# Optimization experiments

Hardware: AMD Instinct MI355X
Metric: run time of the kernel (lower is better)

Reference implementation:

```python
import jax, jax.numpy as jnp
import numpy as np

EPS = 1e-5
NUM_HEADS = 4


def setup_inputs() -> dict:
    key = jax.random.key(0)
    ks = jax.random.split(key, 10)
    B, C, H, W = 16, 512, 32, 32
    s = 1.0 / np.sqrt(C)
    x = jax.random.normal(ks[0], (B, C, H, W), dtype=jnp.float32)
    gn_weight = jnp.ones((C,), jnp.float32)
    gn_bias = jnp.zeros((C,), jnp.float32)
    wq = jax.random.uniform(ks[1], (C, C), jnp.float32, -s, s)
    bq = jax.random.uniform(ks[2], (C,), jnp.float32, -s, s)
    wk = jax.random.uniform(ks[3], (C, C), jnp.float32, -s, s)
    bk = jax.random.uniform(ks[4], (C,), jnp.float32, -s, s)
    wv = jax.random.uniform(ks[5], (C, C), jnp.float32, -s, s)
    bv = jax.random.uniform(ks[6], (C,), jnp.float32, -s, s)
    wo = jax.random.uniform(ks[7], (C, C), jnp.float32, -s, s)
    bo = jax.random.uniform(ks[8], (C,), jnp.float32, -s, s)
    return dict(x=x, gn_weight=gn_weight, gn_bias=gn_bias, wq=wq, bq=bq,
                wk=wk, bk=bk, wv=wv, bv=bv, wo=wo, bo=bo)


def reference(x, gn_weight, gn_bias, wq, bq, wk, bk, wv, bv, wo, bo):
    B, C, H, W = x.shape
    head_size = C // NUM_HEADS

    # GroupNorm(num_groups=1): normalize over (C,H,W) per batch element
    mean = jnp.mean(x, axis=(1, 2, 3), keepdims=True)
    var = jnp.var(x, axis=(1, 2, 3), keepdims=True)
    xn = (x - mean) / jnp.sqrt(var + EPS)
    xn = xn * gn_weight[None, :, None, None] + gn_bias[None, :, None, None]

    # (B, C, H, W) -> (B, S, C) with S = H*W
    seq = xn.reshape(B, C, H * W).transpose(0, 2, 1)

    def heads(y):  # (B, S, C) -> (B, nh, S, hd)
        return y.reshape(B, H * W, NUM_HEADS, head_size).transpose(0, 2, 1, 3)

    q = heads(seq @ wq.T + bq)
    k = heads(seq @ wk.T + bk)
    v = heads(seq @ wv.T + bv)

    scores = jnp.einsum('bhqd,bhkd->bhqk', q, k) / np.sqrt(head_size).astype(np.float32)
    attn = jax.nn.softmax(scores, axis=-1)
    out = jnp.einsum('bhqk,bhkd->bhqd', attn, v)  # (B, nh, S, hd)

    out = out.transpose(0, 2, 1, 3).reshape(B, H * W, C)
    out = out @ wo.T + bo
    out = out.transpose(0, 2, 1).reshape(B, C, H, W)
    return out + x
```

## Files before the change

### kernel.cpp

```cpp
#include <hip/hip_runtime.h>
#include <stdint.h>

#define B_  16
#define C_  512
#define S_  1024
#define NH  4
#define HD  128
#define BS  (B_*S_)

typedef __attribute__((ext_vector_type(8))) short   short8;
typedef __attribute__((ext_vector_type(4))) float   f32x4;
typedef __attribute__((ext_vector_type(4))) unsigned int uint4v;

__device__ __forceinline__ unsigned short f2bf(float f) {
    unsigned u = __float_as_uint(f);
    unsigned r = (u + 0x7fffu + ((u >> 16) & 1u)) >> 16;
    return (unsigned short)r;
}

__device__ __forceinline__ unsigned cvt_pk_bf16(float a, float b) {
    unsigned r;
    asm("v_cvt_pk_bf16_f32 %0, %1, %2" : "=v"(r) : "v"(a), "v"(b));
    return r;
}

__global__ void gn_partial(const float* __restrict__ x, float* __restrict__ part) {
    int b = blockIdx.x, chunk = blockIdx.y;
    const float4* xb = (const float4*)(x + (size_t)b * C_ * S_);
    int base = chunk * 4096 + threadIdx.x;
    float s = 0.f, ss = 0.f;
#pragma unroll
    for (int i = 0; i < 16; ++i) {
        float4 v = xb[base + i * 256];
        s  += v.x + v.y + v.z + v.w;
        ss += v.x*v.x + v.y*v.y + v.z*v.z + v.w*v.w;
    }
    for (int off = 32; off; off >>= 1) { s += __shfl_down(s, off); ss += __shfl_down(ss, off); }
    __shared__ float red[2][4];
    int wv = threadIdx.x >> 6;
    if ((threadIdx.x & 63) == 0) { red[0][wv] = s; red[1][wv] = ss; }
    __syncthreads();
    if (threadIdx.x == 0) {
        s  = red[0][0] + red[0][1] + red[0][2] + red[0][3];
        ss = red[1][0] + red[1][1] + red[1][2] + red[1][3];
        part[(b*32 + chunk)*2 + 0] = s;
        part[(b*32 + chunk)*2 + 1] = ss;
    }
}

__global__ void gn_apply_t(const float* __restrict__ x, const float* __restrict__ part,
                           const float* __restrict__ gw, const float* __restrict__ gb,
                           unsigned short* __restrict__ seq) {
    int st = blockIdx.x, ct = blockIdx.y, b = blockIdx.z;
    float s1 = 0.f, s2 = 0.f;
#pragma unroll
    for (int i = 0; i < 32; ++i) { s1 += part[(b*32+i)*2]; s2 += part[(b*32+i)*2+1]; }
    const float invN = 1.0f / (float)(C_ * S_);
    float mean = s1 * invN;
    float var  = s2 * invN - mean * mean;
    float rstd = rsqrtf(var + 1e-5f);

    __shared__ unsigned short tile[64][72];
    int c0 = ct * 64, s0 = st * 64;
    const float* xb = x + ((size_t)b * C_ + c0) * S_ + s0;
    int tr = threadIdx.x >> 4, tj = (threadIdx.x & 15) * 4;
#pragma unroll
    for (int p = 0; p < 4; ++p) {
        int i = tr + p * 16;
        float w  = gw[c0 + i];
        float bb = gb[c0 + i];
        float4 v = *(const float4*)(xb + (size_t)i * S_ + tj);
        tile[i][tj+0] = f2bf((v.x - mean) * rstd * w + bb);
        tile[i][tj+1] = f2bf((v.y - mean) * rstd * w + bb);
        tile[i][tj+2] = f2bf((v.z - mean) * rstd * w + bb);
        tile[i][tj+3] = f2bf((v.w - mean) * rstd * w + bb);
    }
    __syncthreads();
    int j  = threadIdx.x >> 2;
    int cc = (threadIdx.x & 3) * 16;
    unsigned short tmp[16] __attribute__((aligned(16)));
#pragma unroll
    for (int i = 0; i < 16; ++i) tmp[i] = tile[cc + i][j];
    unsigned short* dst = seq + ((size_t)(b * S_ + s0 + j)) * C_ + c0 + cc;
    *(uint4v*)dst       = *(uint4v*)tmp;
    *(uint4v*)(dst + 8) = *(uint4v*)(tmp + 8);
}

__global__ void cvt_w(const float* __restrict__ wq, const float* __restrict__ wk,
                      const float* __restrict__ wv, const float* __restrict__ wo,
                      unsigned short* __restrict__ wqkv, unsigned short* __restrict__ wobf) {
    int m = blockIdx.y;
    const float* src = (m == 0) ? wq : (m == 1) ? wk : (m == 2) ? wv : wo;
    unsigned short* dst = (m < 3) ? (wqkv + (size_t)m * C_ * C_) : wobf;
    int i = blockIdx.x * 256 + threadIdx.x;
    float4 v = ((const float4*)src)[i];
    unsigned short o[4] __attribute__((aligned(8)));
    o[0] = f2bf(v.x); o[1] = f2bf(v.y); o[2] = f2bf(v.z); o[3] = f2bf(v.w);
    *(unsigned long long*)(dst + (size_t)i * 4) = *(unsigned long long*)o;
}

__device__ __forceinline__ void gemm128_bt(const unsigned short* __restrict__ Ab,
                                           const unsigned short* __restrict__ Bb,
                                           const int K,
                                           unsigned short* lA, unsigned short* lB,
                                           f32x4 acc[4][4]) {
    const int t = threadIdx.x;
    const int w = t >> 6, l = t & 63;
    const int wr = (w >> 1) * 64, wc = (w & 1) * 64;
    const int lrow = l & 15;
    const int lk8  = (l >> 4) * 8;
#pragma unroll
    for (int mi = 0; mi < 4; ++mi)
#pragma unroll
        for (int ni = 0; ni < 4; ++ni)
            acc[mi][ni] = (f32x4){0.f, 0.f, 0.f, 0.f};

    for (int kt = 0; kt < K; kt += 64) {
#pragma unroll
        for (int j = 0; j < 4; ++j) {
            const int lin = j * 256 + t;
            const int row = lin >> 3, ch = lin & 7;
            __builtin_amdgcn_global_load_lds(
                (const __attribute__((address_space(1))) unsigned int*)(Ab + (size_t)row * K + kt + ch * 8),
                (__attribute__((address_space(3))) unsigned int*)(lA + (size_t)(j * 256 + w * 64) * 8),
                16, 0, 0);
        }
#pragma unroll
        for (int j = 0; j < 4; ++j) {
            const int lin = j * 256 + t;
            const int row = lin >> 3, ch = lin & 7;
            __builtin_amdgcn_global_load_lds(
                (const __attribute__((address_space(1))) unsigned int*)(Bb + (size_t)row * K + kt + ch * 8),
                (__attribute__((address_space(3))) unsigned int*)(lB + (size_t)(j * 256 + w * 64) * 8),
                16, 0, 0);
        }
        __syncthreads();
#pragma unroll
        for (int kk = 0; kk < 2; ++kk) {
            short8 af[4], bf[4];
            const int ko = lk8 + kk * 32;
#pragma unroll
            for (int mi = 0; mi < 4; ++mi)
                af[mi] = *(const short8*)&lA[(size_t)(wr + mi * 16 + lrow) * 64 + ko];
#pragma unroll
            for (int ni = 0; ni < 4; ++ni)
                bf[ni] = *(const short8*)&lB[(size_t)(wc + ni * 16 + lrow) * 64 + ko];
#pragma unroll
            for (int mi = 0; mi < 4; ++mi)
#pragma unroll
                for (int ni = 0; ni < 4; ++ni)
                    acc[mi][ni] = __builtin_amdgcn_mfma_f32_16x16x32_bf16(af[mi], bf[ni], acc[mi][ni], 0, 0, 0);
        }
        __syncthreads();
    }
}

__global__ __launch_bounds__(256) void qkv_gemm(
        const unsigned short* __restrict__ seq, const unsigned short* __restrict__ wqkv,
        const float* __restrict__ bq, const float* __restrict__ bk, const float* __restrict__ bv,
        unsigned short* __restrict__ qb, unsigned short* __restrict__ kb, unsigned short* __restrict__ vtb) {
    __shared__ unsigned short sbuf[128 * 136];
    unsigned short* lA = sbuf;
    unsigned short* lB = sbuf + 128 * 64;
    int mb = blockIdx.x, nb = blockIdx.y;
    f32x4 acc[4][4];
    gemm128_bt(seq + (size_t)mb * 128 * C_, wqkv + (size_t)nb * 128 * C_, C_, lA, lB, acc);

    int mat = nb >> 2;
    int cb = (nb & 3) * 128;
    int w = threadIdx.x >> 6, l = threadIdx.x & 63;
    int l15 = l & 15, g = l >> 4;
    int wr = (w >> 1) * 64, wc = (w & 1) * 64;

    if (mat < 2) {
        const float* bias = (mat == 0) ? bq : bk;
        unsigned short* out = (mat == 0) ? qb : kb;
        float oscale = (mat == 0) ? 0.12751879523087253f : 1.0f;
#pragma unroll
        for (int mi = 0; mi < 4; ++mi)
#pragma unroll
            for (int ni = 0; ni < 4; ++ni)
#pragma unroll
                for (int r = 0; r < 4; ++r) {
                    int m = mb * 128 + wr + mi * 16 + g * 4 + r;
                    int c = cb + wc + ni * 16 + l15;
                    int b = m >> 10, s = m & 1023;
                    int h = c >> 7,  d = c & 127;
                    float v = (acc[mi][ni][r] + bias[c]) * oscale;
                    out[(((size_t)(b * NH + h) * S_) + s) * HD + d] = f2bf(v);
                }
    } else {
        int b  = mb >> 3;
        int s0 = (mb & 7) * 128;
        int h  = nb & 3;
#pragma unroll
        for (int mi = 0; mi < 4; ++mi)
#pragma unroll
            for (int ni = 0; ni < 4; ++ni) {
                int dloc = wc + ni * 16 + l15;
                int mloc = wr + mi * 16 + g * 4;
                float bia = bv[h * 128 + dloc];
#pragma unroll
                for (int r = 0; r < 4; ++r)
                    sbuf[dloc * 136 + mloc + r] = f2bf(acc[mi][ni][r] + bia);
            }
        __syncthreads();
        unsigned short* dst = vtb + ((size_t)(b * NH + h)) * HD * S_ + s0;
#pragma unroll
        for (int p = 0; p < 8; ++p) {
            int idx = p * 256 + threadIdx.x;
            int d = idx >> 4, cc = (idx & 15) * 8;
            short8 vv = *(const short8*)&sbuf[d * 136 + cc];
            *(short8*)(dst + (size_t)d * S_ + cc) = vv;
        }
    }
}

__global__ __launch_bounds__(256) void flash_attn(
        const unsigned short* __restrict__ q, const unsigned short* __restrict__ k,
        const unsigned short* __restrict__ vt, unsigned short* __restrict__ o) {
    int bh = blockIdx.x, qblk = blockIdx.y;
    int t = threadIdx.x, w = t >> 6, l = t & 63;
    int l15 = l & 15, g = l >> 4;
    int swz = (l15 & 7) << 1;
    __shared__ unsigned short lK[2][64 * 128];
    __shared__ unsigned short lV[2][128 * 64];
    __shared__ unsigned short lP[4][32 * 64];

    const size_t bh_base = (size_t)bh * S_ * HD;
    int q0 = qblk * 128 + w * 32;

    short8 qa[4], qb_[4];
    const unsigned short* qp = q + bh_base + (size_t)(q0 + l15) * HD + g * 8;
#pragma unroll
    for (int kc = 0; kc < 4; ++kc) {
        qa[kc]  = *(const short8*)(qp + kc * 32);
        qb_[kc] = *(const short8*)(qp + 16 * HD + kc * 32);
    }

    short8 onesf;
#pragma unroll
    for (int i = 0; i < 8; ++i) onesf[i] = (short)0x3F80;

    int ko[4];
#pragma unroll
    for (int nb = 0; nb < 4; ++nb) {
        int row = nb * 16 + l15;
        ko[nb] = row * 256 + ((g ^ row) & 7) * 16;
    }
    int vo[8];
#pragma unroll
    for (int dn = 0; dn < 8; ++dn) {
        int row = dn * 16 + l15;
        vo[dn] = row * 128 + ((g ^ row) & 7) * 16;
    }
    int pw[4], pr[2];
#pragma unroll
    for (int nb = 0; nb < 4; ++nb) pw[nb] = l15 * 128 + (((nb * 4 + g) ^ swz) * 8);
#pragma unroll
    for (int kc = 0; kc < 2; ++kc) pr[kc] = l15 * 128 + (((kc * 8 + g * 2) ^ swz) * 8);

    f32x4 oa[8], ob[8];
#pragma unroll
    for (int i = 0; i < 8; ++i) { oa[i] = (f32x4){0.f,0.f,0.f,0.f}; ob[i] = (f32x4){0.f,0.f,0.f,0.f}; }
    f32x4 lacc_a = (f32x4){0.f,0.f,0.f,0.f}, lacc_b = (f32x4){0.f,0.f,0.f,0.f};
    float m_a = -1e30f, m_b = -1e30f;
    char* myP = (char*)&lP[w][0];

#define STAGE_TILE(buf, kv0_) do {                                                     \
    int kv0s = (kv0_);                                                                 \
    _Pragma("unroll")                                                                  \
    for (int j = 0; j < 4; ++j) {                                                      \
        int lin = j * 256 + t;                                                         \
        int row = lin >> 4, c16 = lin & 15;                                            \
        int sc  = (c16 & 8) | ((c16 ^ row) & 7);                                       \
        __builtin_amdgcn_global_load_lds(                                              \
            (const __attribute__((address_space(1))) unsigned int*)(k + bh_base + (size_t)(kv0s + row) * HD + sc * 8), \
            (__attribute__((address_space(3))) unsigned int*)(&lK[buf][0] + (size_t)(j * 256 + w * 64) * 8), \
            16, 0, 0);                                                                 \
    }                                                                                  \
    _Pragma("unroll")                                                                  \
    for (int j = 0; j < 4; ++j) {                                                      \
        int lin = j * 256 + t;                                                         \
        int row = lin >> 3, c8 = lin & 7;                                              \
        int sc  = (c8 ^ row) & 7;                                                      \
        __builtin_amdgcn_global_load_lds(                                              \
            (const __attribute__((address_space(1))) unsigned int*)(vt + bh_base + (size_t)row * S_ + kv0s + sc * 8), \
            (__attribute__((address_space(3))) unsigned int*)(&lV[buf][0] + (size_t)(j * 256 + w * 64) * 8), \
            16, 0, 0);                                                                 \
    }                                                                                  \
} while (0)

    STAGE_TILE(0, 0);
    __syncthreads();
    int cur = 0;

    for (int kt = 0; kt < 16; ++kt) {
        if (kt < 15) STAGE_TILE(cur ^ 1, (kt + 1) * 64);
        const char* lKc = (const char*)&lK[cur][0];
        const char* lVc = (const char*)&lV[cur][0];

        f32x4 sa[4], sb[4];
#pragma unroll
        for (int nb = 0; nb < 4; ++nb) {
            sa[nb] = (f32x4){0.f,0.f,0.f,0.f};
            sb[nb] = (f32x4){0.f,0.f,0.f,0.f};
        }
        __builtin_amdgcn_s_setprio(1);
#pragma unroll
        for (int kc = 0; kc < 4; ++kc)
#pragma unroll
            for (int nb = 0; nb < 4; ++nb) {
                short8 kf = *(const short8*)(lKc + (ko[nb] ^ (kc << 6)));
                sa[nb] = __builtin_amdgcn_mfma_f32_16x16x32_bf16(kf, qa[kc],  sa[nb], 0, 0, 0);
                sb[nb] = __builtin_amdgcn_mfma_f32_16x16x32_bf16(kf, qb_[kc], sb[nb], 0, 0, 0);
            }
        __builtin_amdgcn_s_setprio(0);

        float mxa = fmaxf(fmaxf(sa[0][0], sa[0][1]), fmaxf(sa[0][2], sa[0][3]));
        float mxb = fmaxf(fmaxf(sb[0][0], sb[0][1]), fmaxf(sb[0][2], sb[0][3]));
#pragma unroll
        for (int nb = 1; nb < 4; ++nb) {
            mxa = fmaxf(mxa, fmaxf(fmaxf(sa[nb][0], sa[nb][1]), fmaxf(sa[nb][2], sa[nb][3])));
            mxb = fmaxf(mxb, fmaxf(fmaxf(sb[nb][0], sb[nb][1]), fmaxf(sb[nb][2], sb[nb][3])));
        }
        mxa = fmaxf(mxa, __shfl_xor(mxa, 16)); mxa = fmaxf(mxa, __shfl_xor(mxa, 32));
        mxb = fmaxf(mxb, __shfl_xor(mxb, 16)); mxb = fmaxf(mxb, __shfl_xor(mxb, 32));

        if (!__all((mxa - m_a <= 8.f) && (mxb - m_b <= 8.f))) {
            float mna = fmaxf(m_a, mxa), mnb = fmaxf(m_b, mxb);
            float ala = exp2f(m_a - mna), alb = exp2f(m_b - mnb);
            m_a = mna; m_b = mnb;
            float a0 = __shfl(ala, g*4+0), a1 = __shfl(ala, g*4+1),
                  a2 = __shfl(ala, g*4+2), a3 = __shfl(ala, g*4+3);
            float b0 = __shfl(alb, g*4+0), b1 = __shfl(alb, g*4+1),
                  b2 = __shfl(alb, g*4+2), b3 = __shfl(alb, g*4+3);
            lacc_a[0] *= a0; lacc_a[1] *= a1; lacc_a[2] *= a2; lacc_a[3] *= a3;
            lacc_b[0] *= b0; lacc_b[1] *= b1; lacc_b[2] *= b2; lacc_b[3] *= b3;
#pragma unroll
            for (int dn = 0; dn < 8; ++dn) {
                oa[dn][0] *= a0; oa[dn][1] *= a1; oa[dn][2] *= a2; oa[dn][3] *= a3;
                ob[dn][0] *= b0; ob[dn][1] *= b1; ob[dn][2] *= b2; ob[dn][3] *= b3;
            }
        }

#pragma unroll
        for (int nb = 0; nb < 4; ++nb) {
            float p0 = exp2f(sa[nb][0] - m_a), p1 = exp2f(sa[nb][1] - m_a);
            float p2 = exp2f(sa[nb][2] - m_a), p3 = exp2f(sa[nb][3] - m_a);
            unsigned d0 = cvt_pk_bf16(p0, p1), d1 = cvt_pk_bf16(p2, p3);
            *(unsigned long long*)(myP + pw[nb]) =
                (unsigned long long)d0 | ((unsigned long long)d1 << 32);
            float r0 = exp2f(sb[nb][0] - m_b), r1 = exp2f(sb[nb][1] - m_b);
            float r2 = exp2f(sb[nb][2] - m_b), r3 = exp2f(sb[nb][3] - m_b);
            unsigned e0 = cvt_pk_bf16(r0, r1), e1 = cvt_pk_bf16(r2, r3);
            *(unsigned long long*)(myP + pw[nb] + 2048) =
                (unsigned long long)e0 | ((unsigned long long)e1 << 32);
        }

        __builtin_amdgcn_s_setprio(1);
#pragma unroll
        for (int kc = 0; kc < 2; ++kc) {
            short8 pa = *(const short8*)(myP + pr[kc]);
            short8 pb = *(const short8*)(myP + pr[kc] + 2048);
            lacc_a = __builtin_amdgcn_mfma_f32_16x16x32_bf16(pa, onesf, lacc_a, 0, 0, 0);
            lacc_b = __builtin_amdgcn_mfma_f32_16x16x32_bf16(pb, onesf, lacc_b, 0, 0, 0);
#pragma unroll
            for (int dn = 0; dn < 8; ++dn) {
                short8 vf = *(const short8*)(lVc + (vo[dn] ^ (kc << 6)));
                oa[dn] = __builtin_amdgcn_mfma_f32_16x16x32_bf16(pa, vf, oa[dn], 0, 0, 0);
                ob[dn] = __builtin_amdgcn_mfma_f32_16x16x32_bf16(pb, vf, ob[dn], 0, 0, 0);
            }
        }
        __builtin_amdgcn_s_setprio(0);
        __syncthreads();
        cur ^= 1;
    }
#undef STAGE_TILE

    float ia0 = 1.0f / lacc_a[0], ia1 = 1.0f / lacc_a[1],
          ia2 = 1.0f / lacc_a[2], ia3 = 1.0f / lacc_a[3];
    float ib0 = 1.0f / lacc_b[0], ib1 = 1.0f / lacc_b[1],
          ib2 = 1.0f / lacc_b[2], ib3 = 1.0f / lacc_b[3];
    int b = bh >> 2, h = bh & 3;
    int sra = q0 + g * 4;
#pragma unroll
    for (int dn = 0; dn < 8; ++dn) {
        int cbase = h * HD + dn * 16 + l15;
        o[((size_t)(b * S_ + sra + 0)) * C_ + cbase]  = f2bf(oa[dn][0] * ia0);
        o[((size_t)(b * S_ + sra + 1)) * C_ + cbase]  = f2bf(oa[dn][1] * ia1);
        o[((size_t)(b * S_ + sra + 2)) * C_ + cbase]  = f2bf(oa[dn][2] * ia2);
        o[((size_t)(b * S_ + sra + 3)) * C_ + cbase]  = f2bf(oa[dn][3] * ia3);
        o[((size_t)(b * S_ + sra + 16)) * C_ + cbase] = f2bf(ob[dn][0] * ib0);
        o[((size_t)(b * S_ + sra + 17)) * C_ + cbase] = f2bf(ob[dn][1] * ib1);
        o[((size_t)(b * S_ + sra + 18)) * C_ + cbase] = f2bf(ob[dn][2] * ib2);
        o[((size_t)(b * S_ + sra + 19)) * C_ + cbase] = f2bf(ob[dn][3] * ib3);
    }
}

__global__ __launch_bounds__(256) void oproj_gemm(
        const unsigned short* __restrict__ wobf, const unsigned short* __restrict__ attn,
        const float* __restrict__ bo, const float* __restrict__ x, float* __restrict__ out) {
    int cbk = blockIdx.x, sb = blockIdx.y, b = blockIdx.z;
    __shared__ unsigned short lA[128 * 64], lB[128 * 64];
    f32x4 acc[4][4];
    gemm128_bt(wobf + (size_t)cbk * 128 * C_,
               attn + ((size_t)b * S_ + sb * 128) * C_, C_, lA, lB, acc);

    int w = threadIdx.x >> 6, l = threadIdx.x & 63;
    int wr = (w >> 1) * 64, wc = (w & 1) * 64;
#pragma unroll
    for (int mi = 0; mi < 4; ++mi)
#pragma unroll
        for (int ni = 0; ni < 4; ++ni)
#pragma unroll
            for (int r = 0; r < 4; ++r) {
                int c = cbk * 128 + wr + mi * 16 + (l >> 4) * 4 + r;
                int s = sb * 128 + wc + ni * 16 + (l & 15);
                size_t off = ((size_t)b * C_ + c) * S_ + s;
                out[off] = acc[mi][ni][r] + bo[c] + x[off];
            }
}

extern "C" void kernel_launch(void* const* d_in, const int* in_sizes, int n_in,
                              void* d_out, int out_size, void* d_ws, size_t ws_size,
                              hipStream_t stream) {
    const float* x  = (const float*)d_in[0];
    const float* gw = (const float*)d_in[1];
    const float* gb = (const float*)d_in[2];
    const float* wq = (const float*)d_in[3];
    const float* bq = (const float*)d_in[4];
    const float* wk = (const float*)d_in[5];
    const float* bk = (const float*)d_in[6];
    const float* wv = (const float*)d_in[7];
    const float* bv = (const float*)d_in[8];
    const float* wo = (const float*)d_in[9];
    const float* bo = (const float*)d_in[10];
    float* out = (float*)d_out;

    char* ws = (char*)d_ws;
    const size_t SEQ_BYTES = (size_t)BS * C_ * 2;
    float* part           = (float*)ws;
    unsigned short* seq   = (unsigned short*)(ws + 4096);
    unsigned short* wqkv  = (unsigned short*)(ws + 4096 + SEQ_BYTES);
    unsigned short* wobf  = (unsigned short*)(ws + 4096 + SEQ_BYTES + 1572864);
    unsigned short* qb    = (unsigned short*)(ws + 4096 + SEQ_BYTES + 1572864 + 524288);
    unsigned short* kb    = qb + 8388608;
    unsigned short* vtb   = kb + 8388608;
    unsigned short* attn  = seq;

    gn_partial<<<dim3(16, 32), 256, 0, stream>>>(x, part);
    gn_apply_t<<<dim3(16, 8, 16), 256, 0, stream>>>(x, part, gw, gb, seq);
    cvt_w<<<dim3(256, 4), 256, 0, stream>>>(wq, wk, wv, wo, wqkv, wobf);
    qkv_gemm<<<dim3(128, 12), 256, 0, stream>>>(seq, wqkv, bq, bk, bv, qb, kb, vtb);
    flash_attn<<<dim3(64, 8), 256, 0, stream>>>(qb, kb, vtb, attn);
    oproj_gemm<<<dim3(4, 8, 16), 256, 0, stream>>>(wobf, attn, bo, x, out);
}
```

Measured before the change: 173.8 us.

## Switch flash attention to 32x32x16 MFMA with register-resident P

Rewrites the attention inner loop to use 32x32x16 bf16 MFMAs, computing S transposed so each lane holds a query column. P is moved into the A-operand layout with v_permlane32_swap instead of going through LDS, and the row sum is accumulated with VALU adds plus a lane swap instead of a ones-MFMA. This removes the per-tile LDS round trip for P and the extra MFMAs used for the denominator, at the cost of more VGPR pressure from the 16-wide accumulators and more cross-lane shuffles during rescaling and the final store.

New measurement: 166.1 us. 4.4% less time.

```diff
diff --git a/kernel.cpp b/kernel.cpp
--- a/kernel.cpp
+++ b/kernel.cpp
@@ -8,9 +8,10 @@
 #define HD  128
 #define BS  (B_*S_)
 
-typedef __attribute__((ext_vector_type(8))) short   short8;
-typedef __attribute__((ext_vector_type(4))) float   f32x4;
-typedef __attribute__((ext_vector_type(4))) unsigned int uint4v;
+typedef __attribute__((ext_vector_type(8)))  short short8;
+typedef __attribute__((ext_vector_type(4)))  float f32x4;
+typedef __attribute__((ext_vector_type(16))) float f32x16;
+typedef __attribute__((ext_vector_type(4)))  unsigned int uint4v;
 
 __device__ __forceinline__ unsigned short f2bf(float f) {
     unsigned u = __float_as_uint(f);
@@ -22,6 +23,12 @@
     unsigned r;
     asm("v_cvt_pk_bf16_f32 %0, %1, %2" : "=v"(r) : "v"(a), "v"(b));
     return r;
+}
+
+__device__ __forceinline__ float xor32_swap(float x, int h) {
+    unsigned a = __float_as_uint(x), b = a;
+    asm volatile("v_permlane32_swap_b32 %0, %1" : "+v"(a), "+v"(b));
+    return __uint_as_float(h ? a : b);
 }
 
 __global__ void gn_partial(const float* __restrict__ x, float* __restrict__ part) {
@@ -221,51 +228,27 @@
         const unsigned short* __restrict__ vt, unsigned short* __restrict__ o) {
     int bh = blockIdx.x, qblk = blockIdx.y;
     int t = threadIdx.x, w = t >> 6, l = t & 63;
-    int l15 = l & 15, g = l >> 4;
-    int swz = (l15 & 7) << 1;
+    int l31 = l & 31, h = l >> 5;
     __shared__ unsigned short lK[2][64 * 128];
     __shared__ unsigned short lV[2][128 * 64];
-    __shared__ unsigned short lP[4][32 * 64];
 
     const size_t bh_base = (size_t)bh * S_ * HD;
     int q0 = qblk * 128 + w * 32;
 
-    short8 qa[4], qb_[4];
-    const unsigned short* qp = q + bh_base + (size_t)(q0 + l15) * HD + g * 8;
-#pragma unroll
-    for (int kc = 0; kc < 4; ++kc) {
-        qa[kc]  = *(const short8*)(qp + kc * 32);
-        qb_[kc] = *(const short8*)(qp + 16 * HD + kc * 32);
-    }
-
-    short8 onesf;
-#pragma unroll
-    for (int i = 0; i < 8; ++i) onesf[i] = (short)0x3F80;
-
-    int ko[4];
-#pragma unroll
-    for (int nb = 0; nb < 4; ++nb) {
-        int row = nb * 16 + l15;
-        ko[nb] = row * 256 + ((g ^ row) & 7) * 16;
-    }
-    int vo[8];
-#pragma unroll
-    for (int dn = 0; dn < 8; ++dn) {
-        int row = dn * 16 + l15;
-        vo[dn] = row * 128 + ((g ^ row) & 7) * 16;
-    }
-    int pw[4], pr[2];
-#pragma unroll
-    for (int nb = 0; nb < 4; ++nb) pw[nb] = l15 * 128 + (((nb * 4 + g) ^ swz) * 8);
-#pragma unroll
-    for (int kc = 0; kc < 2; ++kc) pr[kc] = l15 * 128 + (((kc * 8 + g * 2) ^ swz) * 8);
-
-    f32x4 oa[8], ob[8];
-#pragma unroll
-    for (int i = 0; i < 8; ++i) { oa[i] = (f32x4){0.f,0.f,0.f,0.f}; ob[i] = (f32x4){0.f,0.f,0.f,0.f}; }
-    f32x4 lacc_a = (f32x4){0.f,0.f,0.f,0.f}, lacc_b = (f32x4){0.f,0.f,0.f,0.f};
-    float m_a = -1e30f, m_b = -1e30f;
-    char* myP = (char*)&lP[w][0];
+    short8 qf[8];
+    const unsigned short* qp = q + bh_base + (size_t)(q0 + l31) * HD + h * 8;
+#pragma unroll
+    for (int d = 0; d < 8; ++d) qf[d] = *(const short8*)(qp + d * 16);
+
+    const int kbyte0 = l31 * 256 + (((h ^ l31) & 7) << 4);
+    const int vbyte0 = l31 * 128 + (((h ^ l31) & 7) << 4);
+
+    f32x16 oacc[4];
+#pragma unroll
+    for (int db = 0; db < 4; ++db)
+#pragma unroll
+        for (int r = 0; r < 16; ++r) oacc[db][r] = 0.f;
+    float m_run = -1e30f, l_run = 0.f;
 
 #define STAGE_TILE(buf, kv0_) do {                                                     \
     int kv0s = (kv0_);                                                                 \
@@ -300,76 +283,76 @@
         const char* lKc = (const char*)&lK[cur][0];
         const char* lVc = (const char*)&lV[cur][0];
 
-        f32x4 sa[4], sb[4];
-#pragma unroll
-        for (int nb = 0; nb < 4; ++nb) {
-            sa[nb] = (f32x4){0.f,0.f,0.f,0.f};
-            sb[nb] = (f32x4){0.f,0.f,0.f,0.f};
-        }
+        f32x16 s0, s1;
+#pragma unroll
+        for (int r = 0; r < 16; ++r) { s0[r] = 0.f; s1[r] = 0.f; }
         __builtin_amdgcn_s_setprio(1);
 #pragma unroll
-        for (int kc = 0; kc < 4; ++kc)
-#pragma unroll
-            for (int nb = 0; nb < 4; ++nb) {
-                short8 kf = *(const short8*)(lKc + (ko[nb] ^ (kc << 6)));
-                sa[nb] = __builtin_amdgcn_mfma_f32_16x16x32_bf16(kf, qa[kc],  sa[nb], 0, 0, 0);
-                sb[nb] = __builtin_amdgcn_mfma_f32_16x16x32_bf16(kf, qb_[kc], sb[nb], 0, 0, 0);
+        for (int d = 0; d < 8; ++d) {
+            const char* ka = lKc + (kbyte0 ^ (d << 5));
+            short8 kf0 = *(const short8*)(ka);
+            short8 kf1 = *(const short8*)(ka + 8192);
+            s0 = __builtin_amdgcn_mfma_f32_32x32x16_bf16(kf0, qf[d], s0, 0, 0, 0);
+            s1 = __builtin_amdgcn_mfma_f32_32x32x16_bf16(kf1, qf[d], s1, 0, 0, 0);
+        }
+        __builtin_amdgcn_s_setprio(0);
+
+        float c0 = fmaxf(s0[0], s1[0]), c1 = fmaxf(s0[1], s1[1]);
+        float c2 = fmaxf(s0[2], s1[2]), c3 = fmaxf(s0[3], s1[3]);
+#pragma unroll
+        for (int i = 4; i < 16; i += 4) {
+            c0 = fmaxf(c0, fmaxf(s0[i+0], s1[i+0]));
+            c1 = fmaxf(c1, fmaxf(s0[i+1], s1[i+1]));
+            c2 = fmaxf(c2, fmaxf(s0[i+2], s1[i+2]));
+            c3 = fmaxf(c3, fmaxf(s0[i+3], s1[i+3]));
+        }
+        float mx = fmaxf(fmaxf(c0, c1), fmaxf(c2, c3));
+        mx = fmaxf(mx, xor32_swap(mx, h));
+
+        if (!__all(mx - m_run <= 8.f)) {
+            float mnew  = fmaxf(m_run, mx);
+            float alpha = exp2f(m_run - mnew);
+            m_run = mnew; l_run *= alpha;
+#pragma unroll
+            for (int r = 0; r < 16; ++r) {
+                float ar = __shfl(alpha, (r & 3) + 8 * (r >> 2) + 4 * h);
+                oacc[0][r] *= ar; oacc[1][r] *= ar; oacc[2][r] *= ar; oacc[3][r] *= ar;
             }
-        __builtin_amdgcn_s_setprio(0);
-
-        float mxa = fmaxf(fmaxf(sa[0][0], sa[0][1]), fmaxf(sa[0][2], sa[0][3]));
-        float mxb = fmaxf(fmaxf(sb[0][0], sb[0][1]), fmaxf(sb[0][2], sb[0][3]));
-#pragma unroll
-        for (int nb = 1; nb < 4; ++nb) {
-            mxa = fmaxf(mxa, fmaxf(fmaxf(sa[nb][0], sa[nb][1]), fmaxf(sa[nb][2], sa[nb][3])));
-            mxb = fmaxf(mxb, fmaxf(fmaxf(sb[nb][0], sb[nb][1]), fmaxf(sb[nb][2], sb[nb][3])));
-        }
-        mxa = fmaxf(mxa, __shfl_xor(mxa, 16)); mxa = fmaxf(mxa, __shfl_xor(mxa, 32));
-        mxb = fmaxf(mxb, __shfl_xor(mxb, 16)); mxb = fmaxf(mxb, __shfl_xor(mxb, 32));
-
-        if (!__all((mxa - m_a <= 8.f) && (mxb - m_b <= 8.f))) {
-            float mna = fmaxf(m_a, mxa), mnb = fmaxf(m_b, mxb);
-            float ala = exp2f(m_a - mna), alb = exp2f(m_b - mnb);
-            m_a = mna; m_b = mnb;
-            float a0 = __shfl(ala, g*4+0), a1 = __shfl(ala, g*4+1),
-                  a2 = __shfl(ala, g*4+2), a3 = __shfl(ala, g*4+3);
-            float b0 = __shfl(alb, g*4+0), b1 = __shfl(alb, g*4+1),
-                  b2 = __shfl(alb, g*4+2), b3 = __shfl(alb, g*4+3);
-            lacc_a[0] *= a0; lacc_a[1] *= a1; lacc_a[2] *= a2; lacc_a[3] *= a3;
-            lacc_b[0] *= b0; lacc_b[1] *= b1; lacc_b[2] *= b2; lacc_b[3] *= b3;
-#pragma unroll
-            for (int dn = 0; dn < 8; ++dn) {
-                oa[dn][0] *= a0; oa[dn][1] *= a1; oa[dn][2] *= a2; oa[dn][3] *= a3;
-                ob[dn][0] *= b0; ob[dn][1] *= b1; ob[dn][2] *= b2; ob[dn][3] *= b3;
-            }
-        }
-
-#pragma unroll
-        for (int nb = 0; nb < 4; ++nb) {
-            float p0 = exp2f(sa[nb][0] - m_a), p1 = exp2f(sa[nb][1] - m_a);
-            float p2 = exp2f(sa[nb][2] - m_a), p3 = exp2f(sa[nb][3] - m_a);
-            unsigned d0 = cvt_pk_bf16(p0, p1), d1 = cvt_pk_bf16(p2, p3);
-            *(unsigned long long*)(myP + pw[nb]) =
-                (unsigned long long)d0 | ((unsigned long long)d1 << 32);
-            float r0 = exp2f(sb[nb][0] - m_b), r1 = exp2f(sb[nb][1] - m_b);
-            float r2 = exp2f(sb[nb][2] - m_b), r3 = exp2f(sb[nb][3] - m_b);
-            unsigned e0 = cvt_pk_bf16(r0, r1), e1 = cvt_pk_bf16(r2, r3);
-            *(unsigned long long*)(myP + pw[nb] + 2048) =
-                (unsigned long long)e0 | ((unsigned long long)e1 << 32);
+        }
+
+        float p[32];
+#pragma unroll
+        for (int i = 0; i < 16; ++i) {
+            p[i]      = exp2f(s0[i] - m_run);
+            p[16 + i] = exp2f(s1[i] - m_run);
+        }
+        float a0 = p[0], a1 = p[1], a2 = p[2], a3 = p[3];
+#pragma unroll
+        for (int i = 4; i < 32; i += 4) { a0 += p[i]; a1 += p[i+1]; a2 += p[i+2]; a3 += p[i+3]; }
+        float ps = (a0 + a1) + (a2 + a3);
+        ps += xor32_swap(ps, h);
+        l_run += ps;
+
+        unsigned pr[16];
+#pragma unroll
+        for (int j = 0; j < 16; ++j) pr[j] = cvt_pk_bf16(p[2*j], p[2*j+1]);
+#pragma unroll
+        for (int j4 = 0; j4 < 16; j4 += 4) {
+            asm volatile("v_permlane32_swap_b32 %0, %1" : "+v"(pr[j4+0]), "+v"(pr[j4+2]));
+            asm volatile("v_permlane32_swap_b32 %0, %1" : "+v"(pr[j4+1]), "+v"(pr[j4+3]));
         }
 
         __builtin_amdgcn_s_setprio(1);
 #pragma unroll
-        for (int kc = 0; kc < 2; ++kc) {
-            short8 pa = *(const short8*)(myP + pr[kc]);
-            short8 pb = *(const short8*)(myP + pr[kc] + 2048);
-            lacc_a = __builtin_amdgcn_mfma_f32_16x16x32_bf16(pa, onesf, lacc_a, 0, 0, 0);
-            lacc_b = __builtin_amdgcn_mfma_f32_16x16x32_bf16(pb, onesf, lacc_b, 0, 0, 0);
-#pragma unroll
-            for (int dn = 0; dn < 8; ++dn) {
-                short8 vf = *(const short8*)(lVc + (vo[dn] ^ (kc << 6)));
-                oa[dn] = __builtin_amdgcn_mfma_f32_16x16x32_bf16(pa, vf, oa[dn], 0, 0, 0);
-                ob[dn] = __builtin_amdgcn_mfma_f32_16x16x32_bf16(pb, vf, ob[dn], 0, 0, 0);
+        for (int s_ = 0; s_ < 4; ++s_) {
+            union { unsigned u[4]; short8 v8; } pa;
+            pa.u[0] = pr[s_*4+0]; pa.u[1] = pr[s_*4+1];
+            pa.u[2] = pr[s_*4+2]; pa.u[3] = pr[s_*4+3];
+            const char* va = lVc + (vbyte0 ^ (s_ << 5));
+#pragma unroll
+            for (int db = 0; db < 4; ++db) {
+                short8 vf = *(const short8*)(va + db * 4096);
+                oacc[db] = __builtin_amdgcn_mfma_f32_32x32x16_bf16(pa.v8, vf, oacc[db], 0, 0, 0);
             }
         }
         __builtin_amdgcn_s_setprio(0);
@@ -378,23 +361,17 @@
     }
 #undef STAGE_TILE
 
-    float ia0 = 1.0f / lacc_a[0], ia1 = 1.0f / lacc_a[1],
-          ia2 = 1.0f / lacc_a[2], ia3 = 1.0f / lacc_a[3];
-    float ib0 = 1.0f / lacc_b[0], ib1 = 1.0f / lacc_b[1],
-          ib2 = 1.0f / lacc_b[2], ib3 = 1.0f / lacc_b[3];
-    int b = bh >> 2, h = bh & 3;
-    int sra = q0 + g * 4;
-#pragma unroll
-    for (int dn = 0; dn < 8; ++dn) {
-        int cbase = h * HD + dn * 16 + l15;
-        o[((size_t)(b * S_ + sra + 0)) * C_ + cbase]  = f2bf(oa[dn][0] * ia0);
-        o[((size_t)(b * S_ + sra + 1)) * C_ + cbase]  = f2bf(oa[dn][1] * ia1);
-        o[((size_t)(b * S_ + sra + 2)) * C_ + cbase]  = f2bf(oa[dn][2] * ia2);
-        o[((size_t)(b * S_ + sra + 3)) * C_ + cbase]  = f2bf(oa[dn][3] * ia3);
-        o[((size_t)(b * S_ + sra + 16)) * C_ + cbase] = f2bf(ob[dn][0] * ib0);
-        o[((size_t)(b * S_ + sra + 17)) * C_ + cbase] = f2bf(ob[dn][1] * ib1);
-        o[((size_t)(b * S_ + sra + 18)) * C_ + cbase] = f2bf(ob[dn][2] * ib2);
-        o[((size_t)(b * S_ + sra + 19)) * C_ + cbase] = f2bf(ob[dn][3] * ib3);
+    float linv = 1.0f / l_run;
+    int b = bh >> 2, hh = bh & 3;
+#pragma unroll
+    for (int r = 0; r < 16; ++r) {
+        int qrow = (r & 3) + 8 * (r >> 2) + 4 * h;
+        float li = __shfl(linv, qrow);
+        size_t rowoff = ((size_t)(b * S_ + q0 + qrow)) * C_ + hh * HD + l31;
+        o[rowoff +  0] = f2bf(oacc[0][r] * li);
+        o[rowoff + 32] = f2bf(oacc[1][r] * li);
+        o[rowoff + 64] = f2bf(oacc[2][r] * li);
+        o[rowoff + 96] = f2bf(oacc[3][r] * li);
     }
 }
 
```
